# Kernel optimization log

Hardware: AMD Instinct MI355X
Metric: run time of the kernel (lower is better)

Reference implementation:

```python
import jax, jax.numpy as jnp
import numpy as np

NSTEPS = 4
STEPSIZE = 1.0
B, N_PATCHES, D_LAT = 4, 81920, 32
HIDDEN, D_DYN = 128, 16


def setup_inputs() -> dict:
    key = jax.random.key(0)
    k1, k2, k3, k4 = jax.random.split(key, 4)
    z_old = jax.random.normal(k1, (B, N_PATCHES, D_LAT), dtype=jnp.float32)
    neighbour_list = jax.random.randint(k2, (N_PATCHES, 3), 0, N_PATCHES, dtype=jnp.int32)
    W1 = jax.random.normal(k3, (4 * D_LAT, HIDDEN), dtype=jnp.float32) * (1.0 / np.sqrt(4 * D_LAT))
    b1 = jnp.zeros((HIDDEN,), dtype=jnp.float32)
    W2 = jax.random.normal(k4, (HIDDEN, D_DYN), dtype=jnp.float32) * (1.0 / np.sqrt(HIDDEN))
    b2 = jnp.zeros((D_DYN,), dtype=jnp.float32)
    return {"z_old": z_old, "neighbour_list": neighbour_list, "W1": W1, "b1": b1, "W2": W2, "b2": b2}


def _step(z, neighbour_list, W1, b1, W2, b2):
    # gather neighbour features: (B, n_patches, 3, d_lat)
    neigh = z[:, neighbour_list, :]
    # z_mid: (B, n_patches, d_lat, 4) with slot 0 = self, slots 1..3 = neighbours
    z_mid = jnp.concatenate([z[..., None], jnp.swapaxes(neigh, -1, -2)], axis=-1)
    flat = z_mid.reshape(z.shape[0], z.shape[1], -1)  # (B, n_patches, 4*d_lat)
    h = jnp.tanh(flat @ W1 + b1)
    F_theta = h @ W2 + b2  # (B, n_patches, d_dyn)
    return z.at[:, :, :F_theta.shape[-1]].add(STEPSIZE * F_theta)


def reference(z_old, neighbour_list, W1, b1, W2, b2):
    z = z_old
    for _ in range(NSTEPS):
        z = _step(z, neighbour_list, W1, b1, W2, b2)
    return z
```

## Files before the change

kernel.cpp:

```cpp
#include <hip/hip_runtime.h>

typedef unsigned short u16;
typedef unsigned int u32;
typedef __attribute__((ext_vector_type(8))) short bf16x8;
typedef __attribute__((ext_vector_type(4))) float f32x4;

#define NPATCH 81920
#define NBATCH 4
#define DLAT 32
#define HID 128
#define NROWS (NBATCH * NPATCH)
#define CHUNK 128
#define NCHUNK (NROWS / CHUNK)
#define CPB (NPATCH / CHUNK)
#define SA 136
#define STEPGRID 512

__device__ __forceinline__ u32 f2u(float f) { union { float f; u32 u; } c; c.f = f; return c.u; }
__device__ __forceinline__ float u2f(u32 u) { union { u32 u; float f; } c; c.u = u; return c.f; }
__device__ __forceinline__ u16 bf_rne(float x) {
  u32 u = f2u(x);
  return (u16)((u + 0x7FFFu + ((u >> 16) & 1u)) >> 16);
}

__global__ void prep_kernel(const float* __restrict__ W1, const float* __restrict__ W2,
                            u16* __restrict__ wf, u16* __restrict__ w2t) {
  int t = blockIdx.x * 256 + threadIdx.x;
  if (t < 128 * 128) {
    int kp = t >> 7, n = t & 127;
    int s = kp >> 5, d = kp & 31;
    float v = W1[(d * 4 + s) * HID + n];
    u16 h = bf_rne(v);
    float rem = v - u2f((u32)h << 16);
    u16 l = bf_rne(rem);
    int kg = kp >> 3, j = kp & 7;
    int o = (kg * 128 + n) * 8 + j;
    wf[o] = h;
    wf[16384 + o] = l;
  } else if (t < 128 * 128 + 128 * 16) {
    int uu = t - 128 * 128;
    int k = uu >> 4, o = uu & 15;
    float v = W2[k * 16 + o];
    u16 h = bf_rne(v);
    float rem = v - u2f((u32)h << 16);
    u16 l = bf_rne(rem);
    w2t[o * 128 + k] = h;
    w2t[2048 + o * 128 + k] = l;
  }
}

__global__ __launch_bounds__(256, 2) void step_kernel(
    const float* __restrict__ zin, float* __restrict__ zout,
    const int* __restrict__ nl, const float* __restrict__ b1,
    const float* __restrict__ b2, const u16* __restrict__ wf,
    const u16* __restrict__ w2t) {
  __shared__ __align__(16) u16 AH[CHUNK * SA];
  __shared__ __align__(16) u16 AL[CHUNK * SA];
  __shared__ __align__(16) u16 W2H[16 * SA];
  __shared__ __align__(16) u16 W2L[16 * SA];

  const int tid = threadIdx.x;
  const int lane = tid & 63;
  const int w = tid >> 6;
  const int li = lane & 15;
  const int lg = lane >> 4;

  #pragma unroll
  for (int c = 0; c < 2; ++c) {
    int idx = tid * 2 + c;
    int part = idx >> 8, rest = idx & 255;
    int o = rest >> 4, kc = rest & 15;
    bf16x8 v = *(const bf16x8*)&w2t[part * 2048 + o * 128 + kc * 8];
    u16* dst = part ? W2L : W2H;
    *(bf16x8*)&dst[o * SA + kc * 8] = v;
  }

  bf16x8 WH[2][4], WL[2][4];
  #pragma unroll
  for (int nt = 0; nt < 2; ++nt)
    #pragma unroll
    for (int kt = 0; kt < 4; ++kt) {
      int kg = kt * 4 + lg;
      int n = w * 32 + nt * 16 + li;
      WH[nt][kt] = *(const bf16x8*)&wf[(kg * 128 + n) * 8];
      WL[nt][kt] = *(const bf16x8*)&wf[16384 + (kg * 128 + n) * 8];
    }

  float b1v[2][4];
  #pragma unroll
  for (int nt = 0; nt < 2; ++nt)
    #pragma unroll
    for (int r = 0; r < 4; ++r)
      b1v[nt][r] = b1[w * 32 + nt * 16 + lg * 4 + r];
  float b2v = b2[li];

  for (int chunk = blockIdx.x; chunk < NCHUNK; chunk += gridDim.x) {
    int b = chunk / CPB;
    int row0 = chunk * CHUNK;
    int pbase = row0 - b * NPATCH;
    const float* zb = zin + (size_t)b * NPATCH * DLAT;

    __syncthreads();

    #pragma unroll
    for (int it = 0; it < 2; ++it) {
      int rl = it * 64 + lane;
      int p = pbase + rl;
      int ps = (w == 0) ? p : nl[p * 3 + (w - 1)];
      const float* src = zb + (size_t)ps * DLAT;
      float xs[32];
      #pragma unroll
      for (int q = 0; q < 8; ++q) {
        float4 vv = *(const float4*)&src[q * 4];
        xs[q * 4 + 0] = vv.x; xs[q * 4 + 1] = vv.y;
        xs[q * 4 + 2] = vv.z; xs[q * 4 + 3] = vv.w;
      }
      if (w == 0) {
        float* dsto = zout + (size_t)(row0 + rl) * DLAT;
        *(float4*)&dsto[16] = make_float4(xs[16], xs[17], xs[18], xs[19]);
        *(float4*)&dsto[20] = make_float4(xs[20], xs[21], xs[22], xs[23]);
        *(float4*)&dsto[24] = make_float4(xs[24], xs[25], xs[26], xs[27]);
        *(float4*)&dsto[28] = make_float4(xs[28], xs[29], xs[30], xs[31]);
      }
      int base = rl * SA + w * 32;
      #pragma unroll
      for (int q = 0; q < 4; ++q) {
        bf16x8 hv, lv;
        #pragma unroll
        for (int e = 0; e < 8; ++e) {
          float x = xs[q * 8 + e];
          u16 h = bf_rne(x);
          float rem = x - u2f((u32)h << 16);
          hv[e] = (short)h;
          lv[e] = (short)bf_rne(rem);
        }
        *(bf16x8*)&AH[base + q * 8] = hv;
        *(bf16x8*)&AL[base + q * 8] = lv;
      }
    }
    __syncthreads();

    f32x4 acc[2][8];
    #pragma unroll
    for (int nt = 0; nt < 2; ++nt)
      #pragma unroll
      for (int mt = 0; mt < 8; ++mt)
        acc[nt][mt] = (f32x4){0.f, 0.f, 0.f, 0.f};

    #pragma unroll
    for (int kt = 0; kt < 4; ++kt) {
      #pragma unroll
      for (int mt = 0; mt < 8; ++mt) {
        int off = (mt * 16 + li) * SA + kt * 32 + lg * 8;
        bf16x8 ah = *(const bf16x8*)&AH[off];
        bf16x8 al = *(const bf16x8*)&AL[off];
        #pragma unroll
        for (int nt = 0; nt < 2; ++nt) {
          acc[nt][mt] = __builtin_amdgcn_mfma_f32_16x16x32_bf16(WH[nt][kt], ah, acc[nt][mt], 0, 0, 0);
          acc[nt][mt] = __builtin_amdgcn_mfma_f32_16x16x32_bf16(WH[nt][kt], al, acc[nt][mt], 0, 0, 0);
          acc[nt][mt] = __builtin_amdgcn_mfma_f32_16x16x32_bf16(WL[nt][kt], ah, acc[nt][mt], 0, 0, 0);
        }
      }
    }
    __syncthreads();

    #pragma unroll
    for (int nt = 0; nt < 2; ++nt) {
      #pragma unroll
      for (int mt = 0; mt < 8; ++mt) {
        u32 hw0, hw1, lw0, lw1;
        u16 hh[4], ll[4];
        #pragma unroll
        for (int r = 0; r < 4; ++r) {
          float hval = acc[nt][mt][r] + b1v[nt][r];
          float e = __expf(2.0f * hval);
          float t = 1.0f - 2.0f / (e + 1.0f);
          u16 hb = bf_rne(t);
          float rem = t - u2f((u32)hb << 16);
          hh[r] = hb;
          ll[r] = bf_rne(rem);
        }
        hw0 = (u32)hh[0] | ((u32)hh[1] << 16);
        hw1 = (u32)hh[2] | ((u32)hh[3] << 16);
        lw0 = (u32)ll[0] | ((u32)ll[1] << 16);
        lw1 = (u32)ll[2] | ((u32)ll[3] << 16);
        int m = mt * 16 + li;
        int n = w * 32 + nt * 16 + lg * 4;
        uint2 hv2; hv2.x = hw0; hv2.y = hw1;
        uint2 lv2; lv2.x = lw0; lv2.y = lw1;
        *(uint2*)&AH[m * SA + n] = hv2;
        *(uint2*)&AL[m * SA + n] = lv2;
      }
    }
    __syncthreads();

    f32x4 acc2[2];
    acc2[0] = (f32x4){0.f, 0.f, 0.f, 0.f};
    acc2[1] = (f32x4){0.f, 0.f, 0.f, 0.f};
    #pragma unroll
    for (int kt = 0; kt < 4; ++kt) {
      int woff = li * SA + kt * 32 + lg * 8;
      bf16x8 wh = *(const bf16x8*)&W2H[woff];
      bf16x8 wl = *(const bf16x8*)&W2L[woff];
      #pragma unroll
      for (int mt = 0; mt < 2; ++mt) {
        int off = (w * 32 + mt * 16 + li) * SA + kt * 32 + lg * 8;
        bf16x8 hh = *(const bf16x8*)&AH[off];
        bf16x8 hl = *(const bf16x8*)&AL[off];
        acc2[mt] = __builtin_amdgcn_mfma_f32_16x16x32_bf16(hh, wh, acc2[mt], 0, 0, 0);
        acc2[mt] = __builtin_amdgcn_mfma_f32_16x16x32_bf16(hl, wh, acc2[mt], 0, 0, 0);
        acc2[mt] = __builtin_amdgcn_mfma_f32_16x16x32_bf16(hh, wl, acc2[mt], 0, 0, 0);
      }
    }

    #pragma unroll
    for (int mt = 0; mt < 2; ++mt) {
      #pragma unroll
      for (int r = 0; r < 4; ++r) {
        int rowg = row0 + w * 32 + mt * 16 + lg * 4 + r;
        float F = acc2[mt][r] + b2v;
        size_t oi = (size_t)rowg * DLAT + li;
        zout[oi] = zin[oi] + F;
      }
    }
  }
}

extern "C" void kernel_launch(void* const* d_in, const int* in_sizes, int n_in,
                              void* d_out, int out_size, void* d_ws, size_t ws_size,
                              hipStream_t stream) {
  const float* z_old = (const float*)d_in[0];
  const int* nl = (const int*)d_in[1];
  const float* W1 = (const float*)d_in[2];
  const float* b1 = (const float*)d_in[3];
  const float* W2 = (const float*)d_in[4];
  const float* b2 = (const float*)d_in[5];
  float* out = (float*)d_out;

  u16* wf = (u16*)d_ws;
  u16* w2t = wf + 32768;
  const size_t zoff = 73728;
  const size_t zbytes = (size_t)NROWS * DLAT * sizeof(float);

  prep_kernel<<<72, 256, 0, stream>>>(W1, W2, wf, w2t);

  if (ws_size >= zoff + zbytes) {
    float* zbuf = (float*)((char*)d_ws + zoff);
    step_kernel<<<STEPGRID, 256, 0, stream>>>(z_old, zbuf, nl, b1, b2, wf, w2t);
    step_kernel<<<STEPGRID, 256, 0, stream>>>(zbuf, out, nl, b1, b2, wf, w2t);
    step_kernel<<<STEPGRID, 256, 0, stream>>>(out, zbuf, nl, b1, b2, wf, w2t);
    step_kernel<<<STEPGRID, 256, 0, stream>>>(zbuf, out, nl, b1, b2, wf, w2t);
  } else {
    float* zmut = (float*)d_in[0];
    step_kernel<<<STEPGRID, 256, 0, stream>>>(z_old, out, nl, b1, b2, wf, w2t);
    step_kernel<<<STEPGRID, 256, 0, stream>>>(out, zmut, nl, b1, b2, wf, w2t);
    step_kernel<<<STEPGRID, 256, 0, stream>>>(zmut, out, nl, b1, b2, wf, w2t);
    step_kernel<<<STEPGRID, 256, 0, stream>>>(out, zmut, nl, b1, b2, wf, w2t);
    hipMemcpyAsync(out, zmut, zbytes, hipMemcpyDeviceToDevice, stream);
  }
}
```

Baseline: 395.5 us.

## Store latent state as pre-split bf16 hi/lo and gather via direct-to-LDS loads

Adds a prep pass that converts z into bf16 hi/lo pairs once. The dynamic first 16 dims are kept in ping-pong buffers and the static last 16 in a separate buffer. Each step then gathers the neighbour rows as bf16 straight into LDS with global_load_lds in a k-major layout, which avoids fp32 loads, per-step register conversion and LDS stores. The static half of the fp32 output is written only in the last step. This adds workspace, an extra conversion kernel and a more complex layout, and relies on a larger workspace being available.

```diff
diff --git a/kernel.cpp b/kernel.cpp
--- a/kernel.cpp
+++ b/kernel.cpp
@@ -1,9 +1,11 @@
 #include <hip/hip_runtime.h>
+#include <hip/hip_bf16.h>
 
 typedef unsigned short u16;
 typedef unsigned int u32;
 typedef __attribute__((ext_vector_type(8))) short bf16x8;
 typedef __attribute__((ext_vector_type(4))) float f32x4;
+typedef __attribute__((ext_vector_type(4))) u16 u16x4;
 
 #define NPATCH 81920
 #define NBATCH 4
@@ -13,7 +15,6 @@
 #define CHUNK 128
 #define NCHUNK (NROWS / CHUNK)
 #define CPB (NPATCH / CHUNK)
-#define SA 136
 #define STEPGRID 512
 
 __device__ __forceinline__ u32 f2u(float f) { union { float f; u32 u; } c; c.f = f; return c.u; }
@@ -22,9 +23,222 @@
   u32 u = f2u(x);
   return (u16)((u + 0x7FFFu + ((u >> 16) & 1u)) >> 16);
 }
-
-__global__ void prep_kernel(const float* __restrict__ W1, const float* __restrict__ W2,
-                            u16* __restrict__ wf, u16* __restrict__ w2t) {
+__device__ __forceinline__ u16 f2bf(float x) {
+  union { __hip_bfloat16 b; u16 u; } c; c.b = __float2bfloat16(x); return c.u;
+}
+__device__ __forceinline__ float bf2f(u16 h) {
+  union { __hip_bfloat16 b; u16 u; } c; c.u = h; return __bfloat162float(c.b);
+}
+
+#define GLD(g, l) __builtin_amdgcn_global_load_lds( \
+    (const __attribute__((address_space(1))) void*)(g), \
+    (__attribute__((address_space(3))) void*)(l), 16, 0, 0)
+
+__global__ void prep_w(const float* __restrict__ W1, const float* __restrict__ W2,
+                       u16* __restrict__ wf, u16* __restrict__ w2f) {
+  int t = blockIdx.x * 256 + threadIdx.x;
+  if (t < 128 * 128) {
+    int kp = t >> 7, n = t & 127;
+    int s = kp >> 5, d = kp & 31;
+    float v = W1[(d * 4 + s) * HID + n];
+    u16 h = f2bf(v);
+    u16 l = f2bf(v - bf2f(h));
+    int kg = kp >> 3, j = kp & 7;
+    int o = (kg * 128 + n) * 8 + j;
+    wf[o] = h;
+    wf[16384 + o] = l;
+  } else if (t < 128 * 128 + 2048) {
+    int u = t - 128 * 128;
+    int k = u >> 4, o = u & 15;
+    float v = W2[k * 16 + o];
+    u16 h = f2bf(v);
+    u16 l = f2bf(v - bf2f(h));
+    int kt = k >> 5, lg = (k >> 3) & 3, j = k & 7;
+    int idx = ((kt * 4 + lg) * 16 + o) * 8 + j;
+    w2f[idx] = h;
+    w2f[2048 + idx] = l;
+  }
+}
+
+__global__ void prep_z(const float* __restrict__ z, u16* __restrict__ DA, u16* __restrict__ S) {
+  int t = blockIdx.x * 256 + threadIdx.x;
+  if (t >= NROWS * 8) return;
+  size_t row = (size_t)(t >> 3);
+  int q = t & 7;
+  float4 v = *(const float4*)&z[row * 32 + q * 4];
+  u16 h0 = f2bf(v.x), h1 = f2bf(v.y), h2 = f2bf(v.z), h3 = f2bf(v.w);
+  u16 l0 = f2bf(v.x - bf2f(h0)), l1 = f2bf(v.y - bf2f(h1));
+  u16 l2 = f2bf(v.z - bf2f(h2)), l3 = f2bf(v.w - bf2f(h3));
+  u16* buf = (q < 4) ? DA : S;
+  int qq = q & 3;
+  u16x4 hh = {h0, h1, h2, h3};
+  u16x4 ll = {l0, l1, l2, l3};
+  *(u16x4*)&buf[row * 32 + qq * 4] = hh;
+  *(u16x4*)&buf[row * 32 + 16 + qq * 4] = ll;
+}
+
+template<int FIRST, int LAST>
+__global__ __launch_bounds__(256, 2) void step_kernel(
+    const u16* __restrict__ dIn, u16* __restrict__ dOut,
+    const u16* __restrict__ S, const float* __restrict__ zold,
+    float* __restrict__ zf, const int* __restrict__ nl,
+    const float* __restrict__ b1, const float* __restrict__ b2,
+    const u16* __restrict__ wf, const u16* __restrict__ w2f) {
+  __shared__ __align__(16) u16 AH[4 * 4 * 128 * 8];
+  __shared__ __align__(16) u16 AL[4 * 4 * 128 * 8];
+  __shared__ __align__(16) u16 W2H[2048];
+  __shared__ __align__(16) u16 W2L[2048];
+
+  const int tid = threadIdx.x;
+  const int lane = tid & 63;
+  const int w = tid >> 6;
+  const int li = lane & 15;
+  const int lg = lane >> 4;
+
+  #pragma unroll
+  for (int c = 0; c < 2; ++c) {
+    int idx = tid + c * 256;
+    int part = idx >> 8, slot = idx & 255;
+    u16* dst = part ? W2L : W2H;
+    *(bf16x8*)&dst[slot * 8] = *(const bf16x8*)&w2f[part * 2048 + slot * 8];
+  }
+
+  bf16x8 WH[2][4], WL[2][4];
+  #pragma unroll
+  for (int nt = 0; nt < 2; ++nt)
+    #pragma unroll
+    for (int kt = 0; kt < 4; ++kt) {
+      int kg = kt * 4 + lg;
+      int n = w * 32 + nt * 16 + li;
+      WH[nt][kt] = *(const bf16x8*)&wf[(kg * 128 + n) * 8];
+      WL[nt][kt] = *(const bf16x8*)&wf[16384 + (kg * 128 + n) * 8];
+    }
+
+  float b1v[2][4];
+  #pragma unroll
+  for (int nt = 0; nt < 2; ++nt)
+    #pragma unroll
+    for (int r = 0; r < 4; ++r)
+      b1v[nt][r] = b1[w * 32 + nt * 16 + lg * 4 + r];
+  float b2v = b2[li];
+
+  for (int chunk = blockIdx.x; chunk < NCHUNK; chunk += gridDim.x) {
+    int b = chunk / CPB;
+    int row0 = chunk * CHUNK;
+    int pbase = row0 - b * NPATCH;
+    size_t rb = (size_t)b * NPATCH;
+
+    __syncthreads();
+
+    #pragma unroll
+    for (int it = 0; it < 2; ++it) {
+      int rl = it * 64 + lane;
+      int p = pbase + rl;
+      int ps = p;
+      if (w) ps = nl[p * 3 + (w - 1)];
+      const u16* dsrc = dIn + (rb + (size_t)ps) * 32;
+      const u16* ssrc = S + (rb + (size_t)ps) * 32;
+      int db = ((w * 4) * 128 + it * 64) * 8;
+      GLD(dsrc + 0,  &AH[db + 0 * 1024]);
+      GLD(dsrc + 8,  &AH[db + 1 * 1024]);
+      GLD(ssrc + 0,  &AH[db + 2 * 1024]);
+      GLD(ssrc + 8,  &AH[db + 3 * 1024]);
+      GLD(dsrc + 16, &AL[db + 0 * 1024]);
+      GLD(dsrc + 24, &AL[db + 1 * 1024]);
+      GLD(ssrc + 16, &AL[db + 2 * 1024]);
+      GLD(ssrc + 24, &AL[db + 3 * 1024]);
+    }
+    __syncthreads();
+
+    f32x4 acc[2][8];
+    #pragma unroll
+    for (int nt = 0; nt < 2; ++nt)
+      #pragma unroll
+      for (int mt = 0; mt < 8; ++mt)
+        acc[nt][mt] = (f32x4){0.f, 0.f, 0.f, 0.f};
+
+    #pragma unroll
+    for (int kt = 0; kt < 4; ++kt) {
+      #pragma unroll
+      for (int mt = 0; mt < 8; ++mt) {
+        int off = ((kt * 4 + lg) * 128 + mt * 16 + li) * 8;
+        bf16x8 ah = *(const bf16x8*)&AH[off];
+        bf16x8 al = *(const bf16x8*)&AL[off];
+        #pragma unroll
+        for (int nt = 0; nt < 2; ++nt) {
+          acc[nt][mt] = __builtin_amdgcn_mfma_f32_16x16x32_bf16(WH[nt][kt], ah, acc[nt][mt], 0, 0, 0);
+          acc[nt][mt] = __builtin_amdgcn_mfma_f32_16x16x32_bf16(WH[nt][kt], al, acc[nt][mt], 0, 0, 0);
+          acc[nt][mt] = __builtin_amdgcn_mfma_f32_16x16x32_bf16(WL[nt][kt], ah, acc[nt][mt], 0, 0, 0);
+        }
+      }
+    }
+    __syncthreads();
+
+    #pragma unroll
+    for (int nt = 0; nt < 2; ++nt) {
+      #pragma unroll
+      for (int mt = 0; mt < 8; ++mt) {
+        u16 hh[4], ll[4];
+        #pragma unroll
+        for (int r = 0; r < 4; ++r) {
+          float hval = acc[nt][mt][r] + b1v[nt][r];
+          float e = __expf(2.0f * hval);
+          float t = 1.0f - 2.0f / (e + 1.0f);
+          hh[r] = f2bf(t);
+          ll[r] = f2bf(t - bf2f(hh[r]));
+        }
+        int base = ((w * 4 + nt * 2 + (lg >> 1)) * 128 + mt * 16 + li) * 8 + (lg & 1) * 4;
+        u16x4 hv = {hh[0], hh[1], hh[2], hh[3]};
+        u16x4 lv = {ll[0], ll[1], ll[2], ll[3]};
+        *(u16x4*)&AH[base] = hv;
+        *(u16x4*)&AL[base] = lv;
+      }
+    }
+    __syncthreads();
+
+    f32x4 acc2[2];
+    acc2[0] = (f32x4){0.f, 0.f, 0.f, 0.f};
+    acc2[1] = (f32x4){0.f, 0.f, 0.f, 0.f};
+    #pragma unroll
+    for (int kt = 0; kt < 4; ++kt) {
+      int woff = ((kt * 4 + lg) * 16 + li) * 8;
+      bf16x8 wh = *(const bf16x8*)&W2H[woff];
+      bf16x8 wl = *(const bf16x8*)&W2L[woff];
+      #pragma unroll
+      for (int mt = 0; mt < 2; ++mt) {
+        int off = ((kt * 4 + lg) * 128 + w * 32 + mt * 16 + li) * 8;
+        bf16x8 hh = *(const bf16x8*)&AH[off];
+        bf16x8 hl = *(const bf16x8*)&AL[off];
+        acc2[mt] = __builtin_amdgcn_mfma_f32_16x16x32_bf16(hh, wh, acc2[mt], 0, 0, 0);
+        acc2[mt] = __builtin_amdgcn_mfma_f32_16x16x32_bf16(hl, wh, acc2[mt], 0, 0, 0);
+        acc2[mt] = __builtin_amdgcn_mfma_f32_16x16x32_bf16(hh, wl, acc2[mt], 0, 0, 0);
+      }
+    }
+
+    #pragma unroll
+    for (int mt = 0; mt < 2; ++mt) {
+      #pragma unroll
+      for (int r = 0; r < 4; ++r) {
+        int rowg = row0 + w * 32 + mt * 16 + lg * 4 + r;
+        float F = acc2[mt][r] + b2v;
+        float zi = FIRST ? zold[(size_t)rowg * 32 + li] : zf[(size_t)rowg * 32 + li];
+        float v = zi + F;
+        zf[(size_t)rowg * 32 + li] = v;
+        if (LAST) {
+          zf[(size_t)rowg * 32 + 16 + li] = zold[(size_t)rowg * 32 + 16 + li];
+        } else {
+          u16 h = f2bf(v);
+          dOut[(size_t)rowg * 32 + li] = h;
+          dOut[(size_t)rowg * 32 + 16 + li] = f2bf(v - bf2f(h));
+        }
+      }
+    }
+  }
+}
+
+#define SA 136
+__global__ void prep_old(const float* __restrict__ W1, const float* __restrict__ W2,
+                         u16* __restrict__ wf, u16* __restrict__ w2t) {
   int t = blockIdx.x * 256 + threadIdx.x;
   if (t < 128 * 128) {
     int kp = t >> 7, n = t & 127;
@@ -49,7 +263,7 @@
   }
 }
 
-__global__ __launch_bounds__(256, 2) void step_kernel(
+__global__ __launch_bounds__(256, 2) void step_old(
     const float* __restrict__ zin, float* __restrict__ zout,
     const int* __restrict__ nl, const float* __restrict__ b1,
     const float* __restrict__ b2, const u16* __restrict__ wf,
@@ -58,13 +272,11 @@
   __shared__ __align__(16) u16 AL[CHUNK * SA];
   __shared__ __align__(16) u16 W2H[16 * SA];
   __shared__ __align__(16) u16 W2L[16 * SA];
-
   const int tid = threadIdx.x;
   const int lane = tid & 63;
   const int w = tid >> 6;
   const int li = lane & 15;
   const int lg = lane >> 4;
-
   #pragma unroll
   for (int c = 0; c < 2; ++c) {
     int idx = tid * 2 + c;
@@ -74,7 +286,6 @@
     u16* dst = part ? W2L : W2H;
     *(bf16x8*)&dst[o * SA + kc * 8] = v;
   }
-
   bf16x8 WH[2][4], WL[2][4];
   #pragma unroll
   for (int nt = 0; nt < 2; ++nt)
@@ -85,7 +296,6 @@
       WH[nt][kt] = *(const bf16x8*)&wf[(kg * 128 + n) * 8];
       WL[nt][kt] = *(const bf16x8*)&wf[16384 + (kg * 128 + n) * 8];
     }
-
   float b1v[2][4];
   #pragma unroll
   for (int nt = 0; nt < 2; ++nt)
@@ -93,15 +303,12 @@
     for (int r = 0; r < 4; ++r)
       b1v[nt][r] = b1[w * 32 + nt * 16 + lg * 4 + r];
   float b2v = b2[li];
-
   for (int chunk = blockIdx.x; chunk < NCHUNK; chunk += gridDim.x) {
     int b = chunk / CPB;
     int row0 = chunk * CHUNK;
     int pbase = row0 - b * NPATCH;
     const float* zb = zin + (size_t)b * NPATCH * DLAT;
-
-    __syncthreads();
-
+    __syncthreads();
     #pragma unroll
     for (int it = 0; it < 2; ++it) {
       int rl = it * 64 + lane;
@@ -139,14 +346,12 @@
       }
     }
     __syncthreads();
-
     f32x4 acc[2][8];
     #pragma unroll
     for (int nt = 0; nt < 2; ++nt)
       #pragma unroll
       for (int mt = 0; mt < 8; ++mt)
         acc[nt][mt] = (f32x4){0.f, 0.f, 0.f, 0.f};
-
     #pragma unroll
     for (int kt = 0; kt < 4; ++kt) {
       #pragma unroll
@@ -163,12 +368,10 @@
       }
     }
     __syncthreads();
-
     #pragma unroll
     for (int nt = 0; nt < 2; ++nt) {
       #pragma unroll
       for (int mt = 0; mt < 8; ++mt) {
-        u32 hw0, hw1, lw0, lw1;
         u16 hh[4], ll[4];
         #pragma unroll
         for (int r = 0; r < 4; ++r) {
@@ -180,10 +383,10 @@
           hh[r] = hb;
           ll[r] = bf_rne(rem);
         }
-        hw0 = (u32)hh[0] | ((u32)hh[1] << 16);
-        hw1 = (u32)hh[2] | ((u32)hh[3] << 16);
-        lw0 = (u32)ll[0] | ((u32)ll[1] << 16);
-        lw1 = (u32)ll[2] | ((u32)ll[3] << 16);
+        u32 hw0 = (u32)hh[0] | ((u32)hh[1] << 16);
+        u32 hw1 = (u32)hh[2] | ((u32)hh[3] << 16);
+        u32 lw0 = (u32)ll[0] | ((u32)ll[1] << 16);
+        u32 lw1 = (u32)ll[2] | ((u32)ll[3] << 16);
         int m = mt * 16 + li;
         int n = w * 32 + nt * 16 + lg * 4;
         uint2 hv2; hv2.x = hw0; hv2.y = hw1;
@@ -193,7 +396,6 @@
       }
     }
     __syncthreads();
-
     f32x4 acc2[2];
     acc2[0] = (f32x4){0.f, 0.f, 0.f, 0.f};
     acc2[1] = (f32x4){0.f, 0.f, 0.f, 0.f};
@@ -212,7 +414,6 @@
         acc2[mt] = __builtin_amdgcn_mfma_f32_16x16x32_bf16(hh, wl, acc2[mt], 0, 0, 0);
       }
     }
-
     #pragma unroll
     for (int mt = 0; mt < 2; ++mt) {
       #pragma unroll
@@ -237,25 +438,43 @@
   const float* b2 = (const float*)d_in[5];
   float* out = (float*)d_out;
 
-  u16* wf = (u16*)d_ws;
-  u16* w2t = wf + 32768;
-  const size_t zoff = 73728;
-  const size_t zbytes = (size_t)NROWS * DLAT * sizeof(float);
-
-  prep_kernel<<<72, 256, 0, stream>>>(W1, W2, wf, w2t);
-
-  if (ws_size >= zoff + zbytes) {
-    float* zbuf = (float*)((char*)d_ws + zoff);
-    step_kernel<<<STEPGRID, 256, 0, stream>>>(z_old, zbuf, nl, b1, b2, wf, w2t);
-    step_kernel<<<STEPGRID, 256, 0, stream>>>(zbuf, out, nl, b1, b2, wf, w2t);
-    step_kernel<<<STEPGRID, 256, 0, stream>>>(out, zbuf, nl, b1, b2, wf, w2t);
-    step_kernel<<<STEPGRID, 256, 0, stream>>>(zbuf, out, nl, b1, b2, wf, w2t);
+  const size_t Dbytes = (size_t)NROWS * 32 * sizeof(u16);
+  const size_t need = 73728 + 3 * Dbytes;
+
+  if (ws_size >= need) {
+    u16* wf = (u16*)d_ws;
+    u16* w2f = wf + 32768;
+    char* base = (char*)d_ws + 73728;
+    u16* S  = (u16*)base;
+    u16* DA = (u16*)(base + Dbytes);
+    u16* DB = (u16*)(base + 2 * Dbytes);
+
+    prep_w<<<72, 256, 0, stream>>>(W1, W2, wf, w2f);
+    prep_z<<<(NROWS * 8) / 256, 256, 0, stream>>>(z_old, DA, S);
+
+    step_kernel<1, 0><<<STEPGRID, 256, 0, stream>>>(DA, DB, S, z_old, out, nl, b1, b2, wf, w2f);
+    step_kernel<0, 0><<<STEPGRID, 256, 0, stream>>>(DB, DA, S, z_old, out, nl, b1, b2, wf, w2f);
+    step_kernel<0, 0><<<STEPGRID, 256, 0, stream>>>(DA, DB, S, z_old, out, nl, b1, b2, wf, w2f);
+    step_kernel<0, 1><<<STEPGRID, 256, 0, stream>>>(DB, DA, S, z_old, out, nl, b1, b2, wf, w2f);
   } else {
-    float* zmut = (float*)d_in[0];
-    step_kernel<<<STEPGRID, 256, 0, stream>>>(z_old, out, nl, b1, b2, wf, w2t);
-    step_kernel<<<STEPGRID, 256, 0, stream>>>(out, zmut, nl, b1, b2, wf, w2t);
-    step_kernel<<<STEPGRID, 256, 0, stream>>>(zmut, out, nl, b1, b2, wf, w2t);
-    step_kernel<<<STEPGRID, 256, 0, stream>>>(out, zmut, nl, b1, b2, wf, w2t);
-    hipMemcpyAsync(out, zmut, zbytes, hipMemcpyDeviceToDevice, stream);
-  }
-}
+    u16* wf = (u16*)d_ws;
+    u16* w2t = wf + 32768;
+    const size_t zoff = 73728;
+    const size_t zbytes = (size_t)NROWS * DLAT * sizeof(float);
+    prep_old<<<72, 256, 0, stream>>>(W1, W2, wf, w2t);
+    if (ws_size >= zoff + zbytes) {
+      float* zbuf = (float*)((char*)d_ws + zoff);
+      step_old<<<STEPGRID, 256, 0, stream>>>(z_old, zbuf, nl, b1, b2, wf, w2t);
+      step_old<<<STEPGRID, 256, 0, stream>>>(zbuf, out, nl, b1, b2, wf, w2t);
+      step_old<<<STEPGRID, 256, 0, stream>>>(out, zbuf, nl, b1, b2, wf, w2t);
+      step_old<<<STEPGRID, 256, 0, stream>>>(zbuf, out, nl, b1, b2, wf, w2t);
+    } else {
+      float* zmut = (float*)d_in[0];
+      step_old<<<STEPGRID, 256, 0, stream>>>(z_old, out, nl, b1, b2, wf, w2t);
+      step_old<<<STEPGRID, 256, 0, stream>>>(out, zmut, nl, b1, b2, wf, w2t);
+      step_old<<<STEPGRID, 256, 0, stream>>>(zmut, out, nl, b1, b2, wf, w2t);
+      step_old<<<STEPGRID, 256, 0, stream>>>(out, zmut, nl, b1, b2, wf, w2t);
+      hipMemcpyAsync(out, zmut, zbytes, hipMemcpyDeviceToDevice, stream);
+    }
+  }
+}
```

Result: slower. 418.7 us (+5.9%).

## Pre-split z into bf16 hi/lo buffers and pipeline async LDS gathers

Applied to the files above, without the earlier changes.

Adds a prep pass that splits z into bf16 high/low halves once, so each step gathers pre-split rows straight into LDS with global_load_lds and double buffering. This replaces per-row fp32 loading and in-kernel splitting. The chunk size drops to 64 and the LDS layout becomes k-group-major, which removes padding. The static upper 16 lanes are no longer copied every step and are written only in the last step. The cost is extra workspace and a bf16 side buffer written each step, and the hand-written vmcnt waits are fragile.

```diff
diff --git a/kernel.cpp b/kernel.cpp
--- a/kernel.cpp
+++ b/kernel.cpp
@@ -1,63 +1,98 @@
 #include <hip/hip_runtime.h>
+#include <hip/hip_bf16.h>
 
 typedef unsigned short u16;
 typedef unsigned int u32;
 typedef __attribute__((ext_vector_type(8))) short bf16x8;
 typedef __attribute__((ext_vector_type(4))) float f32x4;
+typedef __attribute__((ext_vector_type(4))) u16 u16x4;
 
 #define NPATCH 81920
 #define NBATCH 4
-#define DLAT 32
+#define NROWS (NBATCH * NPATCH)
 #define HID 128
-#define NROWS (NBATCH * NPATCH)
-#define CHUNK 128
+#define CHUNK 64
 #define NCHUNK (NROWS / CHUNK)
 #define CPB (NPATCH / CHUNK)
-#define SA 136
-#define STEPGRID 512
-
-__device__ __forceinline__ u32 f2u(float f) { union { float f; u32 u; } c; c.f = f; return c.u; }
-__device__ __forceinline__ float u2f(u32 u) { union { u32 u; float f; } c; c.u = u; return c.f; }
-__device__ __forceinline__ u16 bf_rne(float x) {
-  u32 u = f2u(x);
-  return (u16)((u + 0x7FFFu + ((u >> 16) & 1u)) >> 16);
-}
-
-__global__ void prep_kernel(const float* __restrict__ W1, const float* __restrict__ W2,
-                            u16* __restrict__ wf, u16* __restrict__ w2t) {
+#define GSTRIDE 512
+
+__device__ __forceinline__ u16 f2bf(float x) {
+  union { __hip_bfloat16 b; u16 u; } c; c.b = __float2bfloat16(x); return c.u;
+}
+__device__ __forceinline__ float bf2f(u16 h) {
+  union { __hip_bfloat16 b; u16 u; } c; c.u = h; return __bfloat162float(c.b);
+}
+
+#define GLD(g, l) __builtin_amdgcn_global_load_lds( \
+    (const __attribute__((address_space(1))) void*)(g), \
+    (__attribute__((address_space(3))) void*)(l), 16, 0, 0)
+#define SBAR() __builtin_amdgcn_s_barrier()
+#define SCHED0() __builtin_amdgcn_sched_barrier(0)
+
+__global__ void prep_w(const float* __restrict__ W1, const float* __restrict__ W2,
+                       u16* __restrict__ wf, u16* __restrict__ w2f) {
   int t = blockIdx.x * 256 + threadIdx.x;
   if (t < 128 * 128) {
     int kp = t >> 7, n = t & 127;
     int s = kp >> 5, d = kp & 31;
     float v = W1[(d * 4 + s) * HID + n];
-    u16 h = bf_rne(v);
-    float rem = v - u2f((u32)h << 16);
-    u16 l = bf_rne(rem);
+    u16 h = f2bf(v);
+    u16 l = f2bf(v - bf2f(h));
     int kg = kp >> 3, j = kp & 7;
     int o = (kg * 128 + n) * 8 + j;
     wf[o] = h;
     wf[16384 + o] = l;
-  } else if (t < 128 * 128 + 128 * 16) {
-    int uu = t - 128 * 128;
-    int k = uu >> 4, o = uu & 15;
+  } else if (t < 128 * 128 + 2048) {
+    int u = t - 128 * 128;
+    int k = u >> 4, o = u & 15;
     float v = W2[k * 16 + o];
-    u16 h = bf_rne(v);
-    float rem = v - u2f((u32)h << 16);
-    u16 l = bf_rne(rem);
-    w2t[o * 128 + k] = h;
-    w2t[2048 + o * 128 + k] = l;
-  }
-}
-
+    u16 h = f2bf(v);
+    u16 l = f2bf(v - bf2f(h));
+    int kt = k >> 5, lg = (k >> 3) & 3, j = k & 7;
+    int idx = ((kt * 4 + lg) * 16 + o) * 8 + j;
+    w2f[idx] = h;
+    w2f[2048 + idx] = l;
+  }
+}
+
+template<int MERGED>
+__global__ void prep_z(const float* __restrict__ z, u16* __restrict__ A0, u16* __restrict__ B0) {
+  int t = blockIdx.x * 256 + threadIdx.x;
+  if (t >= NROWS * 8) return;
+  size_t row = (size_t)(t >> 3);
+  int q = t & 7;
+  float4 v = *(const float4*)&z[row * 32 + q * 4];
+  u16 h0 = f2bf(v.x), h1 = f2bf(v.y), h2 = f2bf(v.z), h3 = f2bf(v.w);
+  u16 l0 = f2bf(v.x - bf2f(h0)), l1 = f2bf(v.y - bf2f(h1));
+  u16 l2 = f2bf(v.z - bf2f(h2)), l3 = f2bf(v.w - bf2f(h3));
+  u16x4 hh = {h0, h1, h2, h3};
+  u16x4 ll = {l0, l1, l2, l3};
+  int dd = (q & 3) * 4;
+  if (MERGED) {
+    int reg = (q < 4) ? 0 : 32;
+    *(u16x4*)&A0[row * 64 + reg + dd] = hh;
+    *(u16x4*)&A0[row * 64 + reg + 16 + dd] = ll;
+    *(u16x4*)&B0[row * 64 + reg + dd] = hh;
+    *(u16x4*)&B0[row * 64 + reg + 16 + dd] = ll;
+  } else {
+    u16* buf = (q < 4) ? A0 : B0;
+    *(u16x4*)&buf[row * 32 + dd] = hh;
+    *(u16x4*)&buf[row * 32 + 16 + dd] = ll;
+  }
+}
+
+template<int FIRST, int LAST, int MERGED>
 __global__ __launch_bounds__(256, 2) void step_kernel(
-    const float* __restrict__ zin, float* __restrict__ zout,
+    const u16* __restrict__ Zin, u16* __restrict__ Zout,
+    const u16* __restrict__ Sst,
+    const float* __restrict__ zold, float* __restrict__ zf,
     const int* __restrict__ nl, const float* __restrict__ b1,
     const float* __restrict__ b2, const u16* __restrict__ wf,
-    const u16* __restrict__ w2t) {
-  __shared__ __align__(16) u16 AH[CHUNK * SA];
-  __shared__ __align__(16) u16 AL[CHUNK * SA];
-  __shared__ __align__(16) u16 W2H[16 * SA];
-  __shared__ __align__(16) u16 W2L[16 * SA];
+    const u16* __restrict__ w2f) {
+  __shared__ __align__(16) u16 AH[2][16 * 64 * 8];
+  __shared__ __align__(16) u16 AL[2][16 * 64 * 8];
+  __shared__ __align__(16) u16 W2H[2048];
+  __shared__ __align__(16) u16 W2L[2048];
 
   const int tid = threadIdx.x;
   const int lane = tid & 63;
@@ -67,12 +102,10 @@
 
   #pragma unroll
   for (int c = 0; c < 2; ++c) {
-    int idx = tid * 2 + c;
-    int part = idx >> 8, rest = idx & 255;
-    int o = rest >> 4, kc = rest & 15;
-    bf16x8 v = *(const bf16x8*)&w2t[part * 2048 + o * 128 + kc * 8];
+    int idx = tid + c * 256;
+    int part = idx >> 8, slot = idx & 255;
     u16* dst = part ? W2L : W2H;
-    *(bf16x8*)&dst[o * SA + kc * 8] = v;
+    *(bf16x8*)&dst[slot * 8] = *(const bf16x8*)&w2f[part * 2048 + slot * 8];
   }
 
   bf16x8 WH[2][4], WL[2][4];
@@ -94,66 +127,69 @@
       b1v[nt][r] = b1[w * 32 + nt * 16 + lg * 4 + r];
   float b2v = b2[li];
 
-  for (int chunk = blockIdx.x; chunk < NCHUNK; chunk += gridDim.x) {
-    int b = chunk / CPB;
-    int row0 = chunk * CHUNK;
-    int pbase = row0 - b * NPATCH;
-    const float* zb = zin + (size_t)b * NPATCH * DLAT;
-
-    __syncthreads();
-
-    #pragma unroll
-    for (int it = 0; it < 2; ++it) {
-      int rl = it * 64 + lane;
-      int p = pbase + rl;
-      int ps = (w == 0) ? p : nl[p * 3 + (w - 1)];
-      const float* src = zb + (size_t)ps * DLAT;
-      float xs[32];
-      #pragma unroll
-      for (int q = 0; q < 8; ++q) {
-        float4 vv = *(const float4*)&src[q * 4];
-        xs[q * 4 + 0] = vv.x; xs[q * 4 + 1] = vv.y;
-        xs[q * 4 + 2] = vv.z; xs[q * 4 + 3] = vv.w;
-      }
-      if (w == 0) {
-        float* dsto = zout + (size_t)(row0 + rl) * DLAT;
-        *(float4*)&dsto[16] = make_float4(xs[16], xs[17], xs[18], xs[19]);
-        *(float4*)&dsto[20] = make_float4(xs[20], xs[21], xs[22], xs[23]);
-        *(float4*)&dsto[24] = make_float4(xs[24], xs[25], xs[26], xs[27]);
-        *(float4*)&dsto[28] = make_float4(xs[28], xs[29], xs[30], xs[31]);
-      }
-      int base = rl * SA + w * 32;
-      #pragma unroll
-      for (int q = 0; q < 4; ++q) {
-        bf16x8 hv, lv;
-        #pragma unroll
-        for (int e = 0; e < 8; ++e) {
-          float x = xs[q * 8 + e];
-          u16 h = bf_rne(x);
-          float rem = x - u2f((u32)h << 16);
-          hv[e] = (short)h;
-          lv[e] = (short)bf_rne(rem);
-        }
-        *(bf16x8*)&AH[base + q * 8] = hv;
-        *(bf16x8*)&AL[base + q * 8] = lv;
-      }
-    }
-    __syncthreads();
-
-    f32x4 acc[2][8];
+  #define NVLOAD(CN) nl[(((CN) * CHUNK - ((CN) / CPB) * NPATCH) + lane) * 3 + (w - 1)]
+
+  #define STAGE(BUF, CN, NV) do {                                          \
+    int b_ = (CN) / CPB;                                                   \
+    int pb_ = (CN) * CHUNK - b_ * NPATCH;                                  \
+    int ps_ = w ? (NV) : (pb_ + lane);                                     \
+    size_t r_ = (size_t)b_ * NPATCH + (size_t)ps_;                         \
+    u16* ah_ = &AH[BUF][(w * 4) * 512];                                    \
+    u16* al_ = &AL[BUF][(w * 4) * 512];                                    \
+    if (MERGED) {                                                          \
+      const u16* s_ = Zin + r_ * 64;                                       \
+      GLD(s_ + 0,  ah_ + 0);    GLD(s_ + 8,  ah_ + 512);                   \
+      GLD(s_ + 32, ah_ + 1024); GLD(s_ + 40, ah_ + 1536);                  \
+      GLD(s_ + 16, al_ + 0);    GLD(s_ + 24, al_ + 512);                   \
+      GLD(s_ + 48, al_ + 1024); GLD(s_ + 56, al_ + 1536);                  \
+    } else {                                                               \
+      const u16* d_ = Zin + r_ * 32;                                       \
+      const u16* t_ = Sst + r_ * 32;                                       \
+      GLD(d_ + 0,  ah_ + 0);    GLD(d_ + 8,  ah_ + 512);                   \
+      GLD(t_ + 0,  ah_ + 1024); GLD(t_ + 8,  ah_ + 1536);                  \
+      GLD(d_ + 16, al_ + 0);    GLD(d_ + 24, al_ + 512);                   \
+      GLD(t_ + 16, al_ + 1024); GLD(t_ + 24, al_ + 1536);                  \
+    }                                                                      \
+  } while (0)
+
+  int c0 = blockIdx.x;
+  int nv = 0, nv1 = 0;
+  if (w) nv = NVLOAD(c0);
+  {
+    int c1 = c0 + GSTRIDE; if (c1 > NCHUNK - 1) c1 = NCHUNK - 1;
+    if (w) nv1 = NVLOAD(c1);
+  }
+  STAGE(0, c0, nv);
+  asm volatile("s_waitcnt lgkmcnt(0)" ::: "memory");
+  int cur = 0;
+
+  for (int c = c0; c < NCHUNK; c += GSTRIDE) {
+    int cn = c + GSTRIDE;
+    bool hn = cn < NCHUNK;
+    if (hn) STAGE(cur ^ 1, cn, nv1);
+    {
+      int cnn = cn + GSTRIDE; if (cnn > NCHUNK - 1) cnn = NCHUNK - 1;
+      if (w && hn) nv1 = NVLOAD(cnn);
+    }
+    if (!hn)        { asm volatile("s_waitcnt vmcnt(0)" ::: "memory"); }
+    else if (w == 0){ asm volatile("s_waitcnt vmcnt(8)" ::: "memory"); }
+    else            { asm volatile("s_waitcnt vmcnt(9)" ::: "memory"); }
+    SCHED0(); SBAR(); SCHED0();
+
+    f32x4 acc[2][4];
     #pragma unroll
     for (int nt = 0; nt < 2; ++nt)
       #pragma unroll
-      for (int mt = 0; mt < 8; ++mt)
+      for (int mt = 0; mt < 4; ++mt)
         acc[nt][mt] = (f32x4){0.f, 0.f, 0.f, 0.f};
 
     #pragma unroll
     for (int kt = 0; kt < 4; ++kt) {
       #pragma unroll
-      for (int mt = 0; mt < 8; ++mt) {
-        int off = (mt * 16 + li) * SA + kt * 32 + lg * 8;
-        bf16x8 ah = *(const bf16x8*)&AH[off];
-        bf16x8 al = *(const bf16x8*)&AL[off];
+      for (int mt = 0; mt < 4; ++mt) {
+        int off = ((kt * 4 + lg) * 64 + mt * 16 + li) * 8;
+        bf16x8 ah = *(const bf16x8*)&AH[cur][off];
+        bf16x8 al = *(const bf16x8*)&AL[cur][off];
         #pragma unroll
         for (int nt = 0; nt < 2; ++nt) {
           acc[nt][mt] = __builtin_amdgcn_mfma_f32_16x16x32_bf16(WH[nt][kt], ah, acc[nt][mt], 0, 0, 0);
@@ -162,68 +198,70 @@
         }
       }
     }
-    __syncthreads();
+    SCHED0(); SBAR(); SCHED0();
 
     #pragma unroll
     for (int nt = 0; nt < 2; ++nt) {
       #pragma unroll
-      for (int mt = 0; mt < 8; ++mt) {
-        u32 hw0, hw1, lw0, lw1;
+      for (int mt = 0; mt < 4; ++mt) {
         u16 hh[4], ll[4];
         #pragma unroll
         for (int r = 0; r < 4; ++r) {
           float hval = acc[nt][mt][r] + b1v[nt][r];
           float e = __expf(2.0f * hval);
           float t = 1.0f - 2.0f / (e + 1.0f);
-          u16 hb = bf_rne(t);
-          float rem = t - u2f((u32)hb << 16);
-          hh[r] = hb;
-          ll[r] = bf_rne(rem);
+          hh[r] = f2bf(t);
+          ll[r] = f2bf(t - bf2f(hh[r]));
         }
-        hw0 = (u32)hh[0] | ((u32)hh[1] << 16);
-        hw1 = (u32)hh[2] | ((u32)hh[3] << 16);
-        lw0 = (u32)ll[0] | ((u32)ll[1] << 16);
-        lw1 = (u32)ll[2] | ((u32)ll[3] << 16);
-        int m = mt * 16 + li;
-        int n = w * 32 + nt * 16 + lg * 4;
-        uint2 hv2; hv2.x = hw0; hv2.y = hw1;
-        uint2 lv2; lv2.x = lw0; lv2.y = lw1;
-        *(uint2*)&AH[m * SA + n] = hv2;
-        *(uint2*)&AL[m * SA + n] = lv2;
+        int base = ((w * 4 + nt * 2 + (lg >> 1)) * 64 + mt * 16 + li) * 8 + (lg & 1) * 4;
+        u16x4 hv = {hh[0], hh[1], hh[2], hh[3]};
+        u16x4 lv = {ll[0], ll[1], ll[2], ll[3]};
+        *(u16x4*)&AH[cur][base] = hv;
+        *(u16x4*)&AL[cur][base] = lv;
       }
     }
-    __syncthreads();
-
-    f32x4 acc2[2];
-    acc2[0] = (f32x4){0.f, 0.f, 0.f, 0.f};
-    acc2[1] = (f32x4){0.f, 0.f, 0.f, 0.f};
+    asm volatile("s_waitcnt lgkmcnt(0)" ::: "memory");
+    SCHED0(); SBAR(); SCHED0();
+
+    f32x4 acc2 = (f32x4){0.f, 0.f, 0.f, 0.f};
     #pragma unroll
     for (int kt = 0; kt < 4; ++kt) {
-      int woff = li * SA + kt * 32 + lg * 8;
+      int woff = ((kt * 4 + lg) * 16 + li) * 8;
       bf16x8 wh = *(const bf16x8*)&W2H[woff];
       bf16x8 wl = *(const bf16x8*)&W2L[woff];
-      #pragma unroll
-      for (int mt = 0; mt < 2; ++mt) {
-        int off = (w * 32 + mt * 16 + li) * SA + kt * 32 + lg * 8;
-        bf16x8 hh = *(const bf16x8*)&AH[off];
-        bf16x8 hl = *(const bf16x8*)&AL[off];
-        acc2[mt] = __builtin_amdgcn_mfma_f32_16x16x32_bf16(hh, wh, acc2[mt], 0, 0, 0);
-        acc2[mt] = __builtin_amdgcn_mfma_f32_16x16x32_bf16(hl, wh, acc2[mt], 0, 0, 0);
-        acc2[mt] = __builtin_amdgcn_mfma_f32_16x16x32_bf16(hh, wl, acc2[mt], 0, 0, 0);
+      int off = ((kt * 4 + lg) * 64 + w * 16 + li) * 8;
+      bf16x8 hh = *(const bf16x8*)&AH[cur][off];
+      bf16x8 hl = *(const bf16x8*)&AL[cur][off];
+      acc2 = __builtin_amdgcn_mfma_f32_16x16x32_bf16(hh, wh, acc2, 0, 0, 0);
+      acc2 = __builtin_amdgcn_mfma_f32_16x16x32_bf16(hl, wh, acc2, 0, 0, 0);
+      acc2 = __builtin_amdgcn_mfma_f32_16x16x32_bf16(hh, wl, acc2, 0, 0, 0);
+    }
+
+    #pragma unroll
+    for (int r = 0; r < 4; ++r) {
+      int rowg = c * CHUNK + w * 16 + lg * 4 + r;
+      float F = acc2[r] + b2v;
+      float zi = FIRST ? zold[(size_t)rowg * 32 + li] : zf[(size_t)rowg * 32 + li];
+      float v = zi + F;
+      zf[(size_t)rowg * 32 + li] = v;
+      if (LAST) {
+        zf[(size_t)rowg * 32 + 16 + li] = zold[(size_t)rowg * 32 + 16 + li];
+      } else {
+        u16 h = f2bf(v);
+        u16 l = f2bf(v - bf2f(h));
+        if (MERGED) {
+          Zout[(size_t)rowg * 64 + li] = h;
+          Zout[(size_t)rowg * 64 + 16 + li] = l;
+        } else {
+          Zout[(size_t)rowg * 32 + li] = h;
+          Zout[(size_t)rowg * 32 + 16 + li] = l;
+        }
       }
     }
-
-    #pragma unroll
-    for (int mt = 0; mt < 2; ++mt) {
-      #pragma unroll
-      for (int r = 0; r < 4; ++r) {
-        int rowg = row0 + w * 32 + mt * 16 + lg * 4 + r;
-        float F = acc2[mt][r] + b2v;
-        size_t oi = (size_t)rowg * DLAT + li;
-        zout[oi] = zin[oi] + F;
-      }
-    }
-  }
+    cur ^= 1;
+  }
+  #undef STAGE
+  #undef NVLOAD
 }
 
 extern "C" void kernel_launch(void* const* d_in, const int* in_sizes, int n_in,
@@ -237,25 +275,32 @@
   const float* b2 = (const float*)d_in[5];
   float* out = (float*)d_out;
 
+  const size_t wOff = 73728;
+  const size_t DbM = (size_t)NROWS * 64 * sizeof(u16);
+  const size_t DbS = (size_t)NROWS * 32 * sizeof(u16);
+  const size_t needM = wOff + 2 * DbM;
   u16* wf = (u16*)d_ws;
-  u16* w2t = wf + 32768;
-  const size_t zoff = 73728;
-  const size_t zbytes = (size_t)NROWS * DLAT * sizeof(float);
-
-  prep_kernel<<<72, 256, 0, stream>>>(W1, W2, wf, w2t);
-
-  if (ws_size >= zoff + zbytes) {
-    float* zbuf = (float*)((char*)d_ws + zoff);
-    step_kernel<<<STEPGRID, 256, 0, stream>>>(z_old, zbuf, nl, b1, b2, wf, w2t);
-    step_kernel<<<STEPGRID, 256, 0, stream>>>(zbuf, out, nl, b1, b2, wf, w2t);
-    step_kernel<<<STEPGRID, 256, 0, stream>>>(out, zbuf, nl, b1, b2, wf, w2t);
-    step_kernel<<<STEPGRID, 256, 0, stream>>>(zbuf, out, nl, b1, b2, wf, w2t);
+  u16* w2f = wf + 32768;
+  char* base = (char*)d_ws + wOff;
+
+  prep_w<<<72, 256, 0, stream>>>(W1, W2, wf, w2f);
+
+  if (ws_size >= needM) {
+    u16* ZA = (u16*)base;
+    u16* ZB = (u16*)(base + DbM);
+    prep_z<1><<<(NROWS * 8) / 256, 256, 0, stream>>>(z_old, ZA, ZB);
+    step_kernel<1, 0, 1><<<GSTRIDE, 256, 0, stream>>>(ZA, ZB, nullptr, z_old, out, nl, b1, b2, wf, w2f);
+    step_kernel<0, 0, 1><<<GSTRIDE, 256, 0, stream>>>(ZB, ZA, nullptr, z_old, out, nl, b1, b2, wf, w2f);
+    step_kernel<0, 0, 1><<<GSTRIDE, 256, 0, stream>>>(ZA, ZB, nullptr, z_old, out, nl, b1, b2, wf, w2f);
+    step_kernel<0, 1, 1><<<GSTRIDE, 256, 0, stream>>>(ZB, ZA, nullptr, z_old, out, nl, b1, b2, wf, w2f);
   } else {
-    float* zmut = (float*)d_in[0];
-    step_kernel<<<STEPGRID, 256, 0, stream>>>(z_old, out, nl, b1, b2, wf, w2t);
-    step_kernel<<<STEPGRID, 256, 0, stream>>>(out, zmut, nl, b1, b2, wf, w2t);
-    step_kernel<<<STEPGRID, 256, 0, stream>>>(zmut, out, nl, b1, b2, wf, w2t);
-    step_kernel<<<STEPGRID, 256, 0, stream>>>(out, zmut, nl, b1, b2, wf, w2t);
-    hipMemcpyAsync(out, zmut, zbytes, hipMemcpyDeviceToDevice, stream);
-  }
-}
+    u16* S  = (u16*)base;
+    u16* DA = (u16*)(base + DbS);
+    u16* DB = (u16*)(base + 2 * DbS);
+    prep_z<0><<<(NROWS * 8) / 256, 256, 0, stream>>>(z_old, DA, S);
+    step_kernel<1, 0, 0><<<GSTRIDE, 256, 0, stream>>>(DA, DB, S, z_old, out, nl, b1, b2, wf, w2f);
+    step_kernel<0, 0, 0><<<GSTRIDE, 256, 0, stream>>>(DB, DA, S, z_old, out, nl, b1, b2, wf, w2f);
+    step_kernel<0, 0, 0><<<GSTRIDE, 256, 0, stream>>>(DA, DB, S, z_old, out, nl, b1, b2, wf, w2f);
+    step_kernel<0, 1, 0><<<GSTRIDE, 256, 0, stream>>>(DB, DA, S, z_old, out, nl, b1, b2, wf, w2f);
+  }
+}
```

Result: faster. 362.3 us (-8.4%).
